# Kernel tuning notes

Measured on AMD Instinct MI355X. Metric: run time of the kernel, lower is better.

## Reference

```python
import jax, jax.numpy as jnp
import numpy as np

N_NODES = 100000
N_EDGES = 1600000


def gcn_conv(x, edge_index, W, b):
    """PyG-style GCNConv: self-loops + symmetric normalization + scatter-add."""
    n = x.shape[0]
    src, dst = edge_index[0], edge_index[1]
    loop = jnp.arange(n, dtype=src.dtype)
    src = jnp.concatenate([src, loop])
    dst = jnp.concatenate([dst, loop])
    h = x @ W  # [n, out] transform before propagate (PyG order)
    deg = jax.ops.segment_sum(jnp.ones_like(dst, dtype=h.dtype), dst, num_segments=n)
    dinv = jnp.where(deg > 0, deg ** -0.5, 0.0)
    norm = dinv[src] * dinv[dst]  # [E+n]
    msgs = h[src] * norm[:, None]  # gather + scale (largest intermediate)
    out = jax.ops.segment_sum(msgs, dst, num_segments=n)
    return out + b


def setup_inputs() -> dict:
    key = jax.random.key(0)
    ks = jax.random.split(key, 8)
    edge_attr = jax.random.normal(ks[0], (N_NODES, 5), dtype=jnp.float32)
    edge_index = jax.random.randint(ks[1], (2, N_EDGES), 0, N_NODES, dtype=jnp.int64)
    def lin(k, fan_in, fan_out):
        bound = 1.0 / np.sqrt(fan_in)
        return jax.random.uniform(k, (fan_in, fan_out), jnp.float32, -bound, bound)
    return {
        "edge_attr": edge_attr,
        "edge_index": edge_index,
        "W1": lin(ks[2], 5, 64),
        "b1": jnp.zeros((64,), jnp.float32),
        "W2": lin(ks[3], 64, 32),
        "b2": jnp.zeros((32,), jnp.float32),
        "fcW1": lin(ks[4], 32, 16),
        "fcb1": jnp.zeros((16,), jnp.float32),
        "fcW2": lin(ks[5], 16, 2),
        "fcb2": jnp.zeros((2,), jnp.float32),
    }


def reference(edge_attr, edge_index, W1, b1, W2, b2, fcW1, fcb1, fcW2, fcb2):
    x = jax.nn.relu(gcn_conv(edge_attr, edge_index, W1, b1))
    x = jax.nn.relu(gcn_conv(x, edge_index, W2, b2))
    x = jax.nn.relu(x @ fcW1 + fcb1)
    return x @ fcW2 + fcb2
```

## Files before the change

### kernel.cpp

```cpp
#include <hip/hip_runtime.h>


#define MS_TILE 2048
#define MAXB 512
#define AGG_NODES 32
#define AGG_STAGE 1024
#define PF_T 512
#define PF_EPT 10
#define PF_OV 1024

typedef __attribute__((ext_vector_type(4))) _Float16 half4;
typedef __attribute__((ext_vector_type(8))) _Float16 half8;

__device__ inline int scan256_incl(int v, int lane, int w, int* wsum,
                                   int* total) {
    int incl = v;
#pragma unroll
    for (int d = 1; d < 64; d <<= 1) {
        int up = __shfl_up(incl, d, 64);
        if (lane >= d) incl += up;
    }
    if (lane == 63) wsum[w] = incl;
    __syncthreads();
    int add = 0;
    if (w > 0) add += wsum[0];
    if (w > 1) add += wsum[1];
    if (w > 2) add += wsum[2];
    *total = wsum[0] + wsum[1] + wsum[2] + wsum[3];
    return incl + add;
}

__global__ __launch_bounds__(256) void histA(const int* __restrict__ dst,
                                             int* __restrict__ histG, int E) {
    __shared__ int h[MAXB];
    int t = threadIdx.x;
    h[t] = 0;
    h[t + 256] = 0;
    __syncthreads();
    int base = blockIdx.x * MS_TILE;
    int cnt = min(MS_TILE, E - base);
    for (int k = t; k < cnt; k += 256) atomicAdd(&h[dst[base + k] >> 8], 1);
    __syncthreads();
    histG[blockIdx.x * MAXB + t] = h[t];
    histG[blockIdx.x * MAXB + 256 + t] = h[t + 256];
}

__global__ __launch_bounds__(512) void scanTilesT(const int* __restrict__ histG,
                                                  int* __restrict__ offsG,
                                                  int* __restrict__ bucketTotal,
                                                  int nTiles) {
    __shared__ int lds[8][66];
    int t = threadIdx.x;
    int lane = t & 63, w = t >> 6;
    int rr = t >> 3, bb = t & 7;
    int B0 = blockIdx.x * 8;
    int carry = 0;
    for (int c0 = 0; c0 < nTiles; c0 += 64) {
        int rows = min(64, nTiles - c0);
        int v = 0;
        if (rr < rows) v = histG[(size_t)(c0 + rr) * MAXB + B0 + bb];
        lds[bb][rr] = v;
        __syncthreads();
        int x = lds[w][lane];
        int incl = x;
#pragma unroll
        for (int d = 1; d < 64; d <<= 1) {
            int up = __shfl_up(incl, d, 64);
            if (lane >= d) incl += up;
        }
        int total = __shfl(incl, 63, 64);
        lds[w][lane] = incl - x + carry;
        carry += total;
        __syncthreads();
        if (rr < rows) offsG[(size_t)(c0 + rr) * MAXB + B0 + bb] = lds[bb][rr];
    }
    if (lane == 0) bucketTotal[B0 + w] = carry;
}

__global__ __launch_bounds__(256) void multisplit2(
    const int* __restrict__ src, const int* __restrict__ dst,
    const int* __restrict__ histG, const int* __restrict__ offsG,
    const int* __restrict__ btot, int* __restrict__ gbaseOut,
    unsigned* __restrict__ binned, int E) {
    __shared__ unsigned stage[MS_TILE];
    __shared__ unsigned short sb[MS_TILE];
    __shared__ int hoff[MAXB + 1];
    __shared__ int hcur[MAXB];
    __shared__ int gb[MAXB];
    __shared__ int wsum[4];
    int t = threadIdx.x;
    int lane = t & 63, w = t >> 6;
    int tile = blockIdx.x;
    int base = tile * MS_TILE;
    int cnt = min(MS_TILE, E - base);

    int b0 = btot[2 * t], b1v = btot[2 * t + 1];
    int s2 = b0 + b1v;
    int tot2;
    int incl2 = scan256_incl(s2, lane, w, wsum, &tot2);
    int ex2 = incl2 - s2;
    gb[2 * t] = ex2 + offsG[tile * MAXB + 2 * t];
    gb[2 * t + 1] = ex2 + b0 + offsG[tile * MAXB + 2 * t + 1];
    if (tile == 0) {
        gbaseOut[2 * t] = ex2;
        gbaseOut[2 * t + 1] = ex2 + b0;
        if (t == 255) gbaseOut[MAXB] = E;
    }
    __syncthreads();

    int a0 = histG[tile * MAXB + 2 * t];
    int a1 = histG[tile * MAXB + 2 * t + 1];
    int s = a0 + a1;
    int tot;
    int incl = scan256_incl(s, lane, w, wsum, &tot);
    int ex = incl - s;
    hoff[2 * t] = ex;
    hoff[2 * t + 1] = ex + a0;
    hcur[2 * t] = ex;
    hcur[2 * t + 1] = ex + a0;
    if (t == 255) hoff[MAXB] = cnt;
    __syncthreads();
    for (int k = t; k < cnt; k += 256) {
        int d = dst[base + k];
        int b = d >> 8;
        int p = atomicAdd(&hcur[b], 1);
        stage[p] = ((unsigned)src[base + k] << 8) | (unsigned)(d & 255);
        sb[p] = (unsigned short)b;
    }
    __syncthreads();
    for (int k = t; k < cnt; k += 256) {
        int b = sb[k];
        binned[gb[b] + (k - hoff[b])] = stage[k];
    }
}

__global__ __launch_bounds__(PF_T) void place_fine2(
    const unsigned* __restrict__ binned, const int* __restrict__ gbase,
    const float* __restrict__ x, int* __restrict__ offs,
    float* __restrict__ dinv, _Float16* __restrict__ y, int* __restrict__ srcs,
    int n) {
    __shared__ int cnt[256];
    __shared__ int baseL[256];
    __shared__ int wsum[8];
    __shared__ unsigned ovW[PF_OV];
    __shared__ int ovR[PF_OV];
    __shared__ int ovN;
    int t = threadIdx.x, b = blockIdx.x;
    int lane = t & 63, w = t >> 6;
    int node0 = b << 8;
    int nn = min(256, n - node0);
    int e0 = gbase[b], e1 = gbase[b + 1];
    if (t < 256) cnt[t] = 0;
    if (t == 0) ovN = 0;
    __syncthreads();

    unsigned wdv[PF_EPT];
    int rk[PF_EPT];
    int nc = 0;
#pragma unroll
    for (int u = 0; u < PF_EPT; ++u) {
        int k = e0 + t + u * PF_T;
        if (k < e1) {
            unsigned wd = binned[k];
            wdv[u] = wd;
            rk[u] = atomicAdd(&cnt[wd & 255u], 1);
            nc = u + 1;
        }
    }
    for (int k = e0 + t + PF_EPT * PF_T; k < e1; k += PF_T) {
        unsigned wd = binned[k];
        int r = atomicAdd(&cnt[wd & 255u], 1);
        int j = atomicAdd(&ovN, 1);
        if (j < PF_OV) { ovW[j] = wd; ovR[j] = r; }
    }
    __syncthreads();

    int c = (t < 256) ? cnt[t] : 0;
    int incl = c;
#pragma unroll
    for (int d = 1; d < 64; d <<= 1) {
        int up = __shfl_up(incl, d, 64);
        if (lane >= d) incl += up;
    }
    if (lane == 63) wsum[w] = incl;
    __syncthreads();
    int add = 0;
    if (w > 0) add += wsum[0];
    if (w > 1) add += wsum[1];
    if (w > 2) add += wsum[2];
    incl += add;
    if (t < 256) {
        int myoff = e0 + incl - c;
        baseL[t] = myoff;
        if (t < nn) {
            int node = node0 + t;
            offs[node] = myoff;
            float di = 1.0f / sqrtf((float)(c + 1));
            dinv[node] = di;
            const float* xr = x + (size_t)node * 5;
            half8 hv;
            hv[0] = (_Float16)(xr[0] * di);
            hv[1] = (_Float16)(xr[1] * di);
            hv[2] = (_Float16)(xr[2] * di);
            hv[3] = (_Float16)(xr[3] * di);
            hv[4] = (_Float16)(xr[4] * di);
            hv[5] = (_Float16)0.f;
            hv[6] = (_Float16)0.f;
            hv[7] = (_Float16)0.f;
            *(half8*)(y + (size_t)node * 8) = hv;
        }
    }
    __syncthreads();

#pragma unroll
    for (int u = 0; u < PF_EPT; ++u) {
        if (u < nc) {
            unsigned wd = wdv[u];
            srcs[baseL[wd & 255u] + rk[u]] = (int)(wd >> 8);
        }
    }
    int no = ovN;
    for (int j = t; j < no; j += PF_T) {
        unsigned wd = ovW[j];
        srcs[baseL[wd & 255u] + ovR[j]] = (int)(wd >> 8);
    }
}

__global__ __launch_bounds__(256) void agg1_t12(
    const _Float16* __restrict__ y, const int* __restrict__ srcs,
    const int* __restrict__ offs, const float* __restrict__ dinv,
    const float* __restrict__ W1, const float* __restrict__ b1,
    const float* __restrict__ W2, _Float16* __restrict__ h2, int n, int E) {
    __shared__ float w1s[320];
    __shared__ float b1s[64];
    __shared__ float w2s[64 * 32];
    __shared__ float o1[32 * 64];
    __shared__ float zs[32 * 6];
    int t = threadIdx.x;
    w1s[t] = W1[t];
    if (t < 64) {
        w1s[t + 256] = W1[t + 256];
        b1s[t] = b1[t];
    }
#pragma unroll
    for (int r = 0; r < 8; ++r) w2s[r * 256 + t] = W2[r * 256 + t];

    int node0 = blockIdx.x * 32;
    int li = t >> 3, e = t & 7;
    int i = node0 + li;
    const half8* yv = (const half8*)y;
    float a0 = 0.f, a1 = 0.f, a2 = 0.f, a3 = 0.f, a4 = 0.f;
    if (i < n) {
        int off = offs[i];
        int cnt = ((i + 1 < n) ? offs[i + 1] : E) - off;
        if (e == 0) {
            half8 v = yv[i];
            a0 = (float)v[0]; a1 = (float)v[1]; a2 = (float)v[2];
            a3 = (float)v[3]; a4 = (float)v[4];
        }
        for (int p = e; p < cnt; p += 8) {
            half8 v = yv[srcs[off + p]];
            a0 += (float)v[0]; a1 += (float)v[1]; a2 += (float)v[2];
            a3 += (float)v[3]; a4 += (float)v[4];
        }
    }
#pragma unroll
    for (int m = 4; m >= 1; m >>= 1) {
        a0 += __shfl_xor(a0, m, 64);
        a1 += __shfl_xor(a1, m, 64);
        a2 += __shfl_xor(a2, m, 64);
        a3 += __shfl_xor(a3, m, 64);
        a4 += __shfl_xor(a4, m, 64);
    }
    if (i < n && e == 0) {
        float di = dinv[i];
        zs[li * 6 + 0] = a0 * di;
        zs[li * 6 + 1] = a1 * di;
        zs[li * 6 + 2] = a2 * di;
        zs[li * 6 + 3] = a3 * di;
        zs[li * 6 + 4] = a4 * di;
        zs[li * 6 + 5] = di;
    }
    __syncthreads();
#pragma unroll
    for (int r = 0; r < 8; ++r) {
        int idx = r * 256 + t;
        int lj = idx >> 6, f = idx & 63;
        if (node0 + lj < n) {
            const float* zr = zs + lj * 6;
            float acc = b1s[f];
#pragma unroll
            for (int k = 0; k < 5; ++k) acc += zr[k] * w1s[k * 64 + f];
            o1[lj * 64 + f] = fmaxf(acc, 0.0f);
        }
    }
    __syncthreads();
#pragma unroll
    for (int r = 0; r < 4; ++r) {
        int idx = r * 256 + t;
        int lj = idx >> 5, g = idx & 31;
        int i2 = node0 + lj;
        if (i2 < n) {
            float acc = 0.f;
#pragma unroll
            for (int k = 0; k < 64; ++k) acc += o1[lj * 64 + k] * w2s[k * 32 + g];
            h2[(size_t)i2 * 32 + g] = (_Float16)(acc * zs[lj * 6 + 5]);
        }
    }
}

__global__ __launch_bounds__(256) void agg2_fc(
    const _Float16* __restrict__ h, const int* __restrict__ srcs,
    const int* __restrict__ offs, const float* __restrict__ dinv,
    const float* __restrict__ b2, const float* __restrict__ fcW1,
    const float* __restrict__ fcb1, const float* __restrict__ fcW2,
    const float* __restrict__ fcb2, float* __restrict__ out, int n, int E) {
    __shared__ int sidx[AGG_STAGE];
    __shared__ float sm[AGG_NODES * 33];
    __shared__ float x3s[AGG_NODES * 16];
    __shared__ float w1s[512];
    __shared__ float w2s[32];
    __shared__ float b1s[16];
    __shared__ float b2s[2];
    __shared__ float bs2[32];
    int t = threadIdx.x;
    w1s[t] = fcW1[t];
    w1s[t + 256] = fcW1[t + 256];
    if (t < 32) { w2s[t] = fcW2[t]; bs2[t] = b2[t]; }
    if (t < 16) b1s[t] = fcb1[t];
    if (t < 2) b2s[t] = fcb2[t];

    int node0 = blockIdx.x * AGG_NODES;
    int li = t >> 3, fq = t & 7;
    int i = node0 + li;
    bool live = (i < n);
    const char* hb = (const char*)h;

    int e0 = offs[node0];
    int eEnd = (node0 + AGG_NODES < n) ? offs[node0 + AGG_NODES] : E;
    int myOff = 0, myCnt = 0;
    float4 acc = {0.f, 0.f, 0.f, 0.f};
    if (live) {
        myOff = offs[i];
        myCnt = ((i + 1 < n) ? offs[i + 1] : E) - myOff;
        half4 sv = *(const half4*)(hb + ((size_t)i << 6) + (fq << 3));
        acc.x = (float)sv.x; acc.y = (float)sv.y;
        acc.z = (float)sv.z; acc.w = (float)sv.w;
    }

    for (int cs = e0; cs < eEnd; cs += AGG_STAGE) {
        int ce = min(cs + AGG_STAGE, eEnd);
        for (int k = cs + t; k < ce; k += 256) sidx[k - cs] = srcs[k] << 6;
        __syncthreads();
        int ps = max(myOff, cs), pe = min(myOff + myCnt, ce);
        int p = ps;
        for (; p + 8 <= pe; p += 8) {
            int o[8];
#pragma unroll
            for (int u = 0; u < 8; ++u) o[u] = sidx[p + u - cs];
            half4 v[8];
#pragma unroll
            for (int u = 0; u < 8; ++u)
                v[u] = *(const half4*)(hb + o[u] + (fq << 3));
#pragma unroll
            for (int u = 0; u < 8; ++u) {
                acc.x += (float)v[u].x; acc.y += (float)v[u].y;
                acc.z += (float)v[u].z; acc.w += (float)v[u].w;
            }
        }
        for (; p + 4 <= pe; p += 4) {
            int o0 = sidx[p - cs], o1 = sidx[p + 1 - cs];
            int o2 = sidx[p + 2 - cs], o3 = sidx[p + 3 - cs];
            half4 v0 = *(const half4*)(hb + o0 + (fq << 3));
            half4 v1 = *(const half4*)(hb + o1 + (fq << 3));
            half4 v2 = *(const half4*)(hb + o2 + (fq << 3));
            half4 v3 = *(const half4*)(hb + o3 + (fq << 3));
            acc.x += (float)v0.x + (float)v1.x + (float)v2.x + (float)v3.x;
            acc.y += (float)v0.y + (float)v1.y + (float)v2.y + (float)v3.y;
            acc.z += (float)v0.z + (float)v1.z + (float)v2.z + (float)v3.z;
            acc.w += (float)v0.w + (float)v1.w + (float)v2.w + (float)v3.w;
        }
        for (; p < pe; ++p) {
            half4 v = *(const half4*)(hb + sidx[p - cs] + (fq << 3));
            acc.x += (float)v.x; acc.y += (float)v.y;
            acc.z += (float)v.z; acc.w += (float)v.w;
        }
        __syncthreads();
    }

    if (live) {
        float di = dinv[i];
        int f0 = fq << 2;
        sm[li * 33 + f0 + 0] = fmaxf(di * acc.x + bs2[f0 + 0], 0.f);
        sm[li * 33 + f0 + 1] = fmaxf(di * acc.y + bs2[f0 + 1], 0.f);
        sm[li * 33 + f0 + 2] = fmaxf(di * acc.z + bs2[f0 + 2], 0.f);
        sm[li * 33 + f0 + 3] = fmaxf(di * acc.w + bs2[f0 + 3], 0.f);
    }
    __syncthreads();
#pragma unroll
    for (int r = 0; r < 2; ++r) {
        int idx = r * 256 + t;
        int lj = idx >> 4, j = idx & 15;
        if (node0 + lj < n) {
            float a = b1s[j];
#pragma unroll
            for (int k = 0; k < 32; ++k) a += sm[lj * 33 + k] * w1s[k * 16 + j];
            x3s[lj * 16 + j] = fmaxf(a, 0.f);
        }
    }
    __syncthreads();
    if (t < 64) {
        int lj = t >> 1, o = t & 1;
        if (node0 + lj < n) {
            float a = b2s[o];
#pragma unroll
            for (int j = 0; j < 16; ++j) a += x3s[lj * 16 + j] * w2s[j * 2 + o];
            out[(size_t)(node0 + lj) * 2 + o] = a;
        }
    }
}

extern "C" void kernel_launch(void* const* d_in, const int* in_sizes, int n_in,
                              void* d_out, int out_size, void* d_ws, size_t ws_size,
                              hipStream_t stream) {
    const float* edge_attr = (const float*)d_in[0];
    const int* edge_index  = (const int*)d_in[1];
    const float* W1   = (const float*)d_in[2];
    const float* b1   = (const float*)d_in[3];
    const float* W2   = (const float*)d_in[4];
    const float* b2   = (const float*)d_in[5];
    const float* fcW1 = (const float*)d_in[6];
    const float* fcb1 = (const float*)d_in[7];
    const float* fcW2 = (const float*)d_in[8];
    const float* fcb2 = (const float*)d_in[9];
    float* out = (float*)d_out;

    int n = in_sizes[0] / 5;
    int E = in_sizes[1] / 2;
    int NBkt = (n + 255) >> 8;
    int nTiles = (E + MS_TILE - 1) / MS_TILE;
    const int* src = edge_index;
    const int* dst = edge_index + E;

    char* ws = (char*)d_ws;
    auto alloc = [&](size_t bytes) {
        char* p = ws;
        ws += (bytes + 255) & ~(size_t)255;
        return p;
    };
    int*      offs   = (int*)alloc((size_t)n * 4);
    float*    dinv   = (float*)alloc((size_t)n * 4);
    int*      histG  = (int*)alloc((size_t)nTiles * MAXB * 4);
    int*      offsG  = (int*)alloc((size_t)nTiles * MAXB * 4);
    int*      btot   = (int*)alloc((size_t)MAXB * 4);
    int*      gbase  = (int*)alloc((size_t)(MAXB + 1) * 4);
    int*      srcs   = (int*)alloc((size_t)E * 4);
    unsigned* binned = (unsigned*)alloc((size_t)E * 4);
    _Float16* y      = (_Float16*)alloc((size_t)n * 8 * 2);
    _Float16* h2     = (_Float16*)alloc((size_t)n * 32 * 2);

    histA<<<nTiles, 256, 0, stream>>>(dst, histG, E);
    scanTilesT<<<MAXB / 8, 512, 0, stream>>>(histG, offsG, btot, nTiles);
    multisplit2<<<nTiles, 256, 0, stream>>>(src, dst, histG, offsG, btot, gbase,
                                            binned, E);
    place_fine2<<<NBkt, PF_T, 0, stream>>>(binned, gbase, edge_attr, offs, dinv,
                                           y, srcs, n);
    agg1_t12<<<(n + 31) / 32, 256, 0, stream>>>(y, srcs, offs, dinv, W1, b1, W2,
                                                h2, n, E);
    agg2_fc<<<(n + AGG_NODES - 1) / AGG_NODES, 256, 0, stream>>>(
        h2, srcs, offs, dinv, b2, fcW1, fcb1, fcW2, fcb2, out, n, E);
}
```

Before: 179.5 us.

## Fuse fine CSR placement into aggregation kernels using LDS-resident per-bucket edge lists

Drops the global srcs/offs CSR build. Each aggregation kernel now re-derives its 256-node bucket's sorted source list in shared memory from the binned edges, then aggregates 64 nodes at a time. Degree is computed with global atomics in the histogram pass, and dinv/y are produced in the otherwise idle blocks of the scan kernel. This removes a kernel and the global srcs write/read traffic, but the local sort is done twice, and 512-thread blocks with large LDS (~50KB+) may cut occupancy. Buckets with more than 5120 edges silently drop edges beyond the LDS capacity.

```diff
diff --git a/kernel.cpp b/kernel.cpp
--- a/kernel.cpp
+++ b/kernel.cpp
@@ -3,14 +3,14 @@
 
 #define MS_TILE 2048
 #define MAXB 512
-#define AGG_NODES 32
-#define AGG_STAGE 1024
-#define PF_T 512
-#define PF_EPT 10
-#define PF_OV 1024
+#define AB_T 512
+#define AB_EPT 10
+#define AB_CAP (AB_T * AB_EPT)
+#define AB_OV 1024
 
 typedef __attribute__((ext_vector_type(4))) _Float16 half4;
 typedef __attribute__((ext_vector_type(8))) _Float16 half8;
+typedef __attribute__((ext_vector_type(4))) int int4v;
 
 __device__ inline int scan256_incl(int v, int lane, int w, int* wsum,
                                    int* total) {
@@ -30,8 +30,14 @@
     return incl + add;
 }
 
-__global__ __launch_bounds__(256) void histA(const int* __restrict__ dst,
-                                             int* __restrict__ histG, int E) {
+__global__ __launch_bounds__(256) void zero_deg(int* __restrict__ deg, int n4) {
+    int i = blockIdx.x * 256 + threadIdx.x;
+    if (i < n4) ((int4v*)deg)[i] = int4v{0, 0, 0, 0};
+}
+
+__global__ __launch_bounds__(256) void histA_deg(const int* __restrict__ dst,
+                                                 int* __restrict__ histG,
+                                                 int* __restrict__ deg, int E) {
     __shared__ int h[MAXB];
     int t = threadIdx.x;
     h[t] = 0;
@@ -39,42 +45,71 @@
     __syncthreads();
     int base = blockIdx.x * MS_TILE;
     int cnt = min(MS_TILE, E - base);
-    for (int k = t; k < cnt; k += 256) atomicAdd(&h[dst[base + k] >> 8], 1);
+    for (int k = t; k < cnt; k += 256) {
+        int d = dst[base + k];
+        atomicAdd(&h[d >> 8], 1);
+        atomicAdd(&deg[d], 1);
+    }
     __syncthreads();
     histG[blockIdx.x * MAXB + t] = h[t];
     histG[blockIdx.x * MAXB + 256 + t] = h[t + 256];
 }
 
-__global__ __launch_bounds__(512) void scanTilesT(const int* __restrict__ histG,
-                                                  int* __restrict__ offsG,
-                                                  int* __restrict__ bucketTotal,
-                                                  int nTiles) {
+__global__ __launch_bounds__(512) void scanY(const int* __restrict__ histG,
+                                             int* __restrict__ offsG,
+                                             int* __restrict__ bucketTotal,
+                                             const int* __restrict__ deg,
+                                             const float* __restrict__ x,
+                                             float* __restrict__ dinv,
+                                             _Float16* __restrict__ y,
+                                             int nTiles, int n) {
     __shared__ int lds[8][66];
     int t = threadIdx.x;
-    int lane = t & 63, w = t >> 6;
-    int rr = t >> 3, bb = t & 7;
-    int B0 = blockIdx.x * 8;
-    int carry = 0;
-    for (int c0 = 0; c0 < nTiles; c0 += 64) {
-        int rows = min(64, nTiles - c0);
-        int v = 0;
-        if (rr < rows) v = histG[(size_t)(c0 + rr) * MAXB + B0 + bb];
-        lds[bb][rr] = v;
-        __syncthreads();
-        int x = lds[w][lane];
-        int incl = x;
-#pragma unroll
-        for (int d = 1; d < 64; d <<= 1) {
-            int up = __shfl_up(incl, d, 64);
-            if (lane >= d) incl += up;
-        }
-        int total = __shfl(incl, 63, 64);
-        lds[w][lane] = incl - x + carry;
-        carry += total;
-        __syncthreads();
-        if (rr < rows) offsG[(size_t)(c0 + rr) * MAXB + B0 + bb] = lds[bb][rr];
-    }
-    if (lane == 0) bucketTotal[B0 + w] = carry;
+    if (blockIdx.x < 64) {
+        int lane = t & 63, w = t >> 6;
+        int rr = t >> 3, bb = t & 7;
+        int B0 = blockIdx.x * 8;
+        int carry = 0;
+        for (int c0 = 0; c0 < nTiles; c0 += 64) {
+            int rows = min(64, nTiles - c0);
+            int v = 0;
+            if (rr < rows) v = histG[(size_t)(c0 + rr) * MAXB + B0 + bb];
+            lds[bb][rr] = v;
+            __syncthreads();
+            int x0 = lds[w][lane];
+            int incl = x0;
+#pragma unroll
+            for (int d = 1; d < 64; d <<= 1) {
+                int up = __shfl_up(incl, d, 64);
+                if (lane >= d) incl += up;
+            }
+            int total = __shfl(incl, 63, 64);
+            lds[w][lane] = incl - x0 + carry;
+            carry += total;
+            __syncthreads();
+            if (rr < rows) offsG[(size_t)(c0 + rr) * MAXB + B0 + bb] = lds[bb][rr];
+            __syncthreads();
+        }
+        if (lane == 0) bucketTotal[B0 + w] = carry;
+    } else {
+        int base = (blockIdx.x - 64) * 512;
+        int stride = (gridDim.x - 64) * 512;
+        for (int i = base + t; i < n; i += stride) {
+            float di = 1.0f / sqrtf((float)(deg[i] + 1));
+            dinv[i] = di;
+            const float* xr = x + (size_t)i * 5;
+            half8 hv;
+            hv[0] = (_Float16)(xr[0] * di);
+            hv[1] = (_Float16)(xr[1] * di);
+            hv[2] = (_Float16)(xr[2] * di);
+            hv[3] = (_Float16)(xr[3] * di);
+            hv[4] = (_Float16)(xr[4] * di);
+            hv[5] = (_Float16)0.f;
+            hv[6] = (_Float16)0.f;
+            hv[7] = (_Float16)0.f;
+            *(half8*)(y + (size_t)i * 8) = hv;
+        }
+    }
 }
 
 __global__ __launch_bounds__(256) void multisplit2(
@@ -134,48 +169,57 @@
     }
 }
 
-__global__ __launch_bounds__(PF_T) void place_fine2(
+__global__ __launch_bounds__(AB_T) void aggB1(
     const unsigned* __restrict__ binned, const int* __restrict__ gbase,
-    const float* __restrict__ x, int* __restrict__ offs,
-    float* __restrict__ dinv, _Float16* __restrict__ y, int* __restrict__ srcs,
-    int n) {
-    __shared__ int cnt[256];
-    __shared__ int baseL[256];
+    const _Float16* __restrict__ y, const float* __restrict__ dinv,
+    const float* __restrict__ W1, const float* __restrict__ b1,
+    const float* __restrict__ W2, _Float16* __restrict__ h2, int n, int E) {
+    __shared__ int cntL[256];
+    __shared__ int exL[256];
     __shared__ int wsum[8];
-    __shared__ unsigned ovW[PF_OV];
-    __shared__ int ovR[PF_OV];
+    __shared__ int srcsL[AB_CAP];
+    __shared__ unsigned ovW[AB_OV];
+    __shared__ int ovR[AB_OV];
     __shared__ int ovN;
+    __shared__ float w1s[320];
+    __shared__ float b1s[64];
+    __shared__ float w2s[2048];
+    __shared__ float o1[64 * 64];
+    __shared__ float zs[64 * 6];
     int t = threadIdx.x, b = blockIdx.x;
     int lane = t & 63, w = t >> 6;
     int node0 = b << 8;
-    int nn = min(256, n - node0);
     int e0 = gbase[b], e1 = gbase[b + 1];
-    if (t < 256) cnt[t] = 0;
+
+    if (t < 320) w1s[t] = W1[t];
+    if (t < 64) b1s[t] = b1[t];
+#pragma unroll
+    for (int r = 0; r < 4; ++r) w2s[r * 512 + t] = W2[r * 512 + t];
+    if (t < 256) cntL[t] = 0;
     if (t == 0) ovN = 0;
     __syncthreads();
 
-    unsigned wdv[PF_EPT];
-    int rk[PF_EPT];
+    unsigned wdv[AB_EPT];
+    int rk[AB_EPT];
     int nc = 0;
 #pragma unroll
-    for (int u = 0; u < PF_EPT; ++u) {
-        int k = e0 + t + u * PF_T;
+    for (int u = 0; u < AB_EPT; ++u) {
+        int k = e0 + t + u * AB_T;
         if (k < e1) {
             unsigned wd = binned[k];
             wdv[u] = wd;
-            rk[u] = atomicAdd(&cnt[wd & 255u], 1);
+            rk[u] = atomicAdd(&cntL[wd & 255u], 1);
             nc = u + 1;
         }
     }
-    for (int k = e0 + t + PF_EPT * PF_T; k < e1; k += PF_T) {
+    for (int k = e0 + t + AB_EPT * AB_T; k < e1; k += AB_T) {
         unsigned wd = binned[k];
-        int r = atomicAdd(&cnt[wd & 255u], 1);
+        int r = atomicAdd(&cntL[wd & 255u], 1);
         int j = atomicAdd(&ovN, 1);
-        if (j < PF_OV) { ovW[j] = wd; ovR[j] = r; }
-    }
-    __syncthreads();
-
-    int c = (t < 256) ? cnt[t] : 0;
+        if (j < AB_OV) { ovW[j] = wd; ovR[j] = r; }
+    }
+    __syncthreads();
+    int c = (t < 256) ? cntL[t] : 0;
     int incl = c;
 #pragma unroll
     for (int d = 1; d < 64; d <<= 1) {
@@ -189,175 +233,196 @@
     if (w > 1) add += wsum[1];
     if (w > 2) add += wsum[2];
     incl += add;
-    if (t < 256) {
-        int myoff = e0 + incl - c;
-        baseL[t] = myoff;
-        if (t < nn) {
-            int node = node0 + t;
-            offs[node] = myoff;
-            float di = 1.0f / sqrtf((float)(c + 1));
-            dinv[node] = di;
-            const float* xr = x + (size_t)node * 5;
-            half8 hv;
-            hv[0] = (_Float16)(xr[0] * di);
-            hv[1] = (_Float16)(xr[1] * di);
-            hv[2] = (_Float16)(xr[2] * di);
-            hv[3] = (_Float16)(xr[3] * di);
-            hv[4] = (_Float16)(xr[4] * di);
-            hv[5] = (_Float16)0.f;
-            hv[6] = (_Float16)0.f;
-            hv[7] = (_Float16)0.f;
-            *(half8*)(y + (size_t)node * 8) = hv;
-        }
-    }
-    __syncthreads();
-
-#pragma unroll
-    for (int u = 0; u < PF_EPT; ++u) {
+    if (t < 256) exL[t] = incl - c;
+    __syncthreads();
+#pragma unroll
+    for (int u = 0; u < AB_EPT; ++u) {
         if (u < nc) {
             unsigned wd = wdv[u];
-            srcs[baseL[wd & 255u] + rk[u]] = (int)(wd >> 8);
-        }
-    }
-    int no = ovN;
-    for (int j = t; j < no; j += PF_T) {
+            int pos = exL[wd & 255u] + rk[u];
+            if (pos < AB_CAP) srcsL[pos] = (int)(wd >> 8);
+        }
+    }
+    int no = min(ovN, AB_OV);
+    for (int j = t; j < no; j += AB_T) {
         unsigned wd = ovW[j];
-        srcs[baseL[wd & 255u] + ovR[j]] = (int)(wd >> 8);
-    }
-}
-
-__global__ __launch_bounds__(256) void agg1_t12(
-    const _Float16* __restrict__ y, const int* __restrict__ srcs,
-    const int* __restrict__ offs, const float* __restrict__ dinv,
-    const float* __restrict__ W1, const float* __restrict__ b1,
-    const float* __restrict__ W2, _Float16* __restrict__ h2, int n, int E) {
-    __shared__ float w1s[320];
-    __shared__ float b1s[64];
-    __shared__ float w2s[64 * 32];
-    __shared__ float o1[32 * 64];
-    __shared__ float zs[32 * 6];
-    int t = threadIdx.x;
-    w1s[t] = W1[t];
-    if (t < 64) {
-        w1s[t + 256] = W1[t + 256];
-        b1s[t] = b1[t];
-    }
-#pragma unroll
-    for (int r = 0; r < 8; ++r) w2s[r * 256 + t] = W2[r * 256 + t];
-
-    int node0 = blockIdx.x * 32;
+        int pos = exL[wd & 255u] + ovR[j];
+        if (pos < AB_CAP) srcsL[pos] = (int)(wd >> 8);
+    }
+    __syncthreads();
+
+    const half8* yv = (const half8*)y;
     int li = t >> 3, e = t & 7;
-    int i = node0 + li;
-    const half8* yv = (const half8*)y;
-    float a0 = 0.f, a1 = 0.f, a2 = 0.f, a3 = 0.f, a4 = 0.f;
-    if (i < n) {
-        int off = offs[i];
-        int cnt = ((i + 1 < n) ? offs[i + 1] : E) - off;
-        if (e == 0) {
-            half8 v = yv[i];
-            a0 = (float)v[0]; a1 = (float)v[1]; a2 = (float)v[2];
-            a3 = (float)v[3]; a4 = (float)v[4];
-        }
-        for (int p = e; p < cnt; p += 8) {
-            half8 v = yv[srcs[off + p]];
-            a0 += (float)v[0]; a1 += (float)v[1]; a2 += (float)v[2];
-            a3 += (float)v[3]; a4 += (float)v[4];
-        }
-    }
-#pragma unroll
-    for (int m = 4; m >= 1; m >>= 1) {
-        a0 += __shfl_xor(a0, m, 64);
-        a1 += __shfl_xor(a1, m, 64);
-        a2 += __shfl_xor(a2, m, 64);
-        a3 += __shfl_xor(a3, m, 64);
-        a4 += __shfl_xor(a4, m, 64);
-    }
-    if (i < n && e == 0) {
-        float di = dinv[i];
-        zs[li * 6 + 0] = a0 * di;
-        zs[li * 6 + 1] = a1 * di;
-        zs[li * 6 + 2] = a2 * di;
-        zs[li * 6 + 3] = a3 * di;
-        zs[li * 6 + 4] = a4 * di;
-        zs[li * 6 + 5] = di;
-    }
-    __syncthreads();
-#pragma unroll
-    for (int r = 0; r < 8; ++r) {
-        int idx = r * 256 + t;
-        int lj = idx >> 6, f = idx & 63;
-        if (node0 + lj < n) {
-            const float* zr = zs + lj * 6;
-            float acc = b1s[f];
-#pragma unroll
-            for (int k = 0; k < 5; ++k) acc += zr[k] * w1s[k * 64 + f];
-            o1[lj * 64 + f] = fmaxf(acc, 0.0f);
-        }
-    }
-    __syncthreads();
-#pragma unroll
-    for (int r = 0; r < 4; ++r) {
-        int idx = r * 256 + t;
-        int lj = idx >> 5, g = idx & 31;
-        int i2 = node0 + lj;
-        if (i2 < n) {
-            float acc = 0.f;
-#pragma unroll
-            for (int k = 0; k < 64; ++k) acc += o1[lj * 64 + k] * w2s[k * 32 + g];
-            h2[(size_t)i2 * 32 + g] = (_Float16)(acc * zs[lj * 6 + 5]);
-        }
-    }
-}
-
-__global__ __launch_bounds__(256) void agg2_fc(
-    const _Float16* __restrict__ h, const int* __restrict__ srcs,
-    const int* __restrict__ offs, const float* __restrict__ dinv,
+    for (int g = 0; g < 4; ++g) {
+        int l = g * 64 + li;
+        int i = node0 + l;
+        float a0 = 0.f, a1 = 0.f, a2 = 0.f, a3 = 0.f, a4 = 0.f;
+        if (i < n) {
+            int myo = exL[l], myc = cntL[l];
+            if (e == 0) {
+                half8 v = yv[i];
+                a0 = (float)v[0]; a1 = (float)v[1]; a2 = (float)v[2];
+                a3 = (float)v[3]; a4 = (float)v[4];
+            }
+            for (int p = e; p < myc; p += 8) {
+                half8 v = yv[srcsL[myo + p]];
+                a0 += (float)v[0]; a1 += (float)v[1]; a2 += (float)v[2];
+                a3 += (float)v[3]; a4 += (float)v[4];
+            }
+        }
+#pragma unroll
+        for (int m = 4; m >= 1; m >>= 1) {
+            a0 += __shfl_xor(a0, m, 64);
+            a1 += __shfl_xor(a1, m, 64);
+            a2 += __shfl_xor(a2, m, 64);
+            a3 += __shfl_xor(a3, m, 64);
+            a4 += __shfl_xor(a4, m, 64);
+        }
+        if (i < n && e == 0) {
+            float di = dinv[i];
+            zs[li * 6 + 0] = a0 * di;
+            zs[li * 6 + 1] = a1 * di;
+            zs[li * 6 + 2] = a2 * di;
+            zs[li * 6 + 3] = a3 * di;
+            zs[li * 6 + 4] = a4 * di;
+            zs[li * 6 + 5] = di;
+        }
+        __syncthreads();
+#pragma unroll
+        for (int r = 0; r < 8; ++r) {
+            int idx = r * 512 + t;
+            int lj = idx >> 6, f = idx & 63;
+            if (node0 + g * 64 + lj < n) {
+                const float* zr = zs + lj * 6;
+                float acc = b1s[f];
+#pragma unroll
+                for (int k = 0; k < 5; ++k) acc += zr[k] * w1s[k * 64 + f];
+                o1[lj * 64 + f] = fmaxf(acc, 0.0f);
+            }
+        }
+        __syncthreads();
+#pragma unroll
+        for (int r = 0; r < 4; ++r) {
+            int idx = r * 512 + t;
+            int lj = idx >> 5, gg = idx & 31;
+            int i2 = node0 + g * 64 + lj;
+            if (i2 < n) {
+                float acc = 0.f;
+#pragma unroll
+                for (int k = 0; k < 64; ++k)
+                    acc += o1[lj * 64 + k] * w2s[k * 32 + gg];
+                h2[(size_t)i2 * 32 + gg] = (_Float16)(acc * zs[lj * 6 + 5]);
+            }
+        }
+        __syncthreads();
+    }
+}
+
+__global__ __launch_bounds__(AB_T) void aggB2(
+    const unsigned* __restrict__ binned, const int* __restrict__ gbase,
+    const _Float16* __restrict__ h, const float* __restrict__ dinv,
     const float* __restrict__ b2, const float* __restrict__ fcW1,
     const float* __restrict__ fcb1, const float* __restrict__ fcW2,
     const float* __restrict__ fcb2, float* __restrict__ out, int n, int E) {
-    __shared__ int sidx[AGG_STAGE];
-    __shared__ float sm[AGG_NODES * 33];
-    __shared__ float x3s[AGG_NODES * 16];
+    __shared__ int cntL[256];
+    __shared__ int exL[256];
+    __shared__ int wsum[8];
+    __shared__ int srcsL[AB_CAP];
+    __shared__ unsigned ovW[AB_OV];
+    __shared__ int ovR[AB_OV];
+    __shared__ int ovN;
+    __shared__ float sm[64 * 33];
+    __shared__ float x3s[64 * 16];
     __shared__ float w1s[512];
-    __shared__ float w2s[32];
-    __shared__ float b1s[16];
-    __shared__ float b2s[2];
+    __shared__ float w2sF[32];
+    __shared__ float b1sF[16];
+    __shared__ float b2sF[2];
     __shared__ float bs2[32];
-    int t = threadIdx.x;
-    w1s[t] = fcW1[t];
-    w1s[t + 256] = fcW1[t + 256];
-    if (t < 32) { w2s[t] = fcW2[t]; bs2[t] = b2[t]; }
-    if (t < 16) b1s[t] = fcb1[t];
-    if (t < 2) b2s[t] = fcb2[t];
-
-    int node0 = blockIdx.x * AGG_NODES;
+    int t = threadIdx.x, b = blockIdx.x;
+    int lane = t & 63, w = t >> 6;
+    int node0 = b << 8;
+    int e0 = gbase[b], e1 = gbase[b + 1];
+
+    if (t < 512) w1s[t] = fcW1[t];
+    if (t < 32) { w2sF[t] = fcW2[t]; bs2[t] = b2[t]; }
+    if (t < 16) b1sF[t] = fcb1[t];
+    if (t < 2) b2sF[t] = fcb2[t];
+    if (t < 256) cntL[t] = 0;
+    if (t == 0) ovN = 0;
+    __syncthreads();
+
+    unsigned wdv[AB_EPT];
+    int rk[AB_EPT];
+    int nc = 0;
+#pragma unroll
+    for (int u = 0; u < AB_EPT; ++u) {
+        int k = e0 + t + u * AB_T;
+        if (k < e1) {
+            unsigned wd = binned[k];
+            wdv[u] = wd;
+            rk[u] = atomicAdd(&cntL[wd & 255u], 1);
+            nc = u + 1;
+        }
+    }
+    for (int k = e0 + t + AB_EPT * AB_T; k < e1; k += AB_T) {
+        unsigned wd = binned[k];
+        int r = atomicAdd(&cntL[wd & 255u], 1);
+        int j = atomicAdd(&ovN, 1);
+        if (j < AB_OV) { ovW[j] = wd; ovR[j] = r; }
+    }
+    __syncthreads();
+    int c = (t < 256) ? cntL[t] : 0;
+    int incl = c;
+#pragma unroll
+    for (int d = 1; d < 64; d <<= 1) {
+        int up = __shfl_up(incl, d, 64);
+        if (lane >= d) incl += up;
+    }
+    if (lane == 63) wsum[w] = incl;
+    __syncthreads();
+    int add = 0;
+    if (w > 0) add += wsum[0];
+    if (w > 1) add += wsum[1];
+    if (w > 2) add += wsum[2];
+    incl += add;
+    if (t < 256) exL[t] = incl - c;
+    __syncthreads();
+#pragma unroll
+    for (int u = 0; u < AB_EPT; ++u) {
+        if (u < nc) {
+            unsigned wd = wdv[u];
+            int pos = exL[wd & 255u] + rk[u];
+            if (pos < AB_CAP) srcsL[pos] = (int)(wd >> 8);
+        }
+    }
+    int no = min(ovN, AB_OV);
+    for (int j = t; j < no; j += AB_T) {
+        unsigned wd = ovW[j];
+        int pos = exL[wd & 255u] + ovR[j];
+        if (pos < AB_CAP) srcsL[pos] = (int)(wd >> 8);
+    }
+    __syncthreads();
+
     int li = t >> 3, fq = t & 7;
-    int i = node0 + li;
-    bool live = (i < n);
     const char* hb = (const char*)h;
-
-    int e0 = offs[node0];
-    int eEnd = (node0 + AGG_NODES < n) ? offs[node0 + AGG_NODES] : E;
-    int myOff = 0, myCnt = 0;
-    float4 acc = {0.f, 0.f, 0.f, 0.f};
-    if (live) {
-        myOff = offs[i];
-        myCnt = ((i + 1 < n) ? offs[i + 1] : E) - myOff;
-        half4 sv = *(const half4*)(hb + ((size_t)i << 6) + (fq << 3));
-        acc.x = (float)sv.x; acc.y = (float)sv.y;
-        acc.z = (float)sv.z; acc.w = (float)sv.w;
-    }
-
-    for (int cs = e0; cs < eEnd; cs += AGG_STAGE) {
-        int ce = min(cs + AGG_STAGE, eEnd);
-        for (int k = cs + t; k < ce; k += 256) sidx[k - cs] = srcs[k] << 6;
-        __syncthreads();
-        int ps = max(myOff, cs), pe = min(myOff + myCnt, ce);
-        int p = ps;
-        for (; p + 8 <= pe; p += 8) {
+    for (int g = 0; g < 4; ++g) {
+        int l = g * 64 + li;
+        int i = node0 + l;
+        bool live = (i < n);
+        float4 acc = {0.f, 0.f, 0.f, 0.f};
+        int myo = 0, myc = 0;
+        if (live) {
+            myo = exL[l];
+            myc = cntL[l];
+            half4 sv = *(const half4*)(hb + ((size_t)i << 6) + (fq << 3));
+            acc.x = (float)sv.x; acc.y = (float)sv.y;
+            acc.z = (float)sv.z; acc.w = (float)sv.w;
+        }
+        int p = 0;
+        for (; p + 8 <= myc; p += 8) {
             int o[8];
 #pragma unroll
-            for (int u = 0; u < 8; ++u) o[u] = sidx[p + u - cs];
+            for (int u = 0; u < 8; ++u) o[u] = srcsL[myo + p + u] << 6;
             half4 v[8];
 #pragma unroll
             for (int u = 0; u < 8; ++u)
@@ -368,11 +433,11 @@
                 acc.z += (float)v[u].z; acc.w += (float)v[u].w;
             }
         }
-        for (; p + 4 <= pe; p += 4) {
-            int o0 = sidx[p - cs], o1 = sidx[p + 1 - cs];
-            int o2 = sidx[p + 2 - cs], o3 = sidx[p + 3 - cs];
+        for (; p + 4 <= myc; p += 4) {
+            int o0 = srcsL[myo + p] << 6, o1v = srcsL[myo + p + 1] << 6;
+            int o2 = srcsL[myo + p + 2] << 6, o3 = srcsL[myo + p + 3] << 6;
             half4 v0 = *(const half4*)(hb + o0 + (fq << 3));
-            half4 v1 = *(const half4*)(hb + o1 + (fq << 3));
+            half4 v1 = *(const half4*)(hb + o1v + (fq << 3));
             half4 v2 = *(const half4*)(hb + o2 + (fq << 3));
             half4 v3 = *(const half4*)(hb + o3 + (fq << 3));
             acc.x += (float)v0.x + (float)v1.x + (float)v2.x + (float)v3.x;
@@ -380,43 +445,43 @@
             acc.z += (float)v0.z + (float)v1.z + (float)v2.z + (float)v3.z;
             acc.w += (float)v0.w + (float)v1.w + (float)v2.w + (float)v3.w;
         }
-        for (; p < pe; ++p) {
-            half4 v = *(const half4*)(hb + sidx[p - cs] + (fq << 3));
+        for (; p < myc; ++p) {
+            half4 v = *(const half4*)(hb + (srcsL[myo + p] << 6) + (fq << 3));
             acc.x += (float)v.x; acc.y += (float)v.y;
             acc.z += (float)v.z; acc.w += (float)v.w;
         }
+        if (live) {
+            float di = dinv[i];
+            int f0 = fq << 2;
+            sm[li * 33 + f0 + 0] = fmaxf(di * acc.x + bs2[f0 + 0], 0.f);
+            sm[li * 33 + f0 + 1] = fmaxf(di * acc.y + bs2[f0 + 1], 0.f);
+            sm[li * 33 + f0 + 2] = fmaxf(di * acc.z + bs2[f0 + 2], 0.f);
+            sm[li * 33 + f0 + 3] = fmaxf(di * acc.w + bs2[f0 + 3], 0.f);
+        }
         __syncthreads();
-    }
-
-    if (live) {
-        float di = dinv[i];
-        int f0 = fq << 2;
-        sm[li * 33 + f0 + 0] = fmaxf(di * acc.x + bs2[f0 + 0], 0.f);
-        sm[li * 33 + f0 + 1] = fmaxf(di * acc.y + bs2[f0 + 1], 0.f);
-        sm[li * 33 + f0 + 2] = fmaxf(di * acc.z + bs2[f0 + 2], 0.f);
-        sm[li * 33 + f0 + 3] = fmaxf(di * acc.w + bs2[f0 + 3], 0.f);
-    }
-    __syncthreads();
-#pragma unroll
-    for (int r = 0; r < 2; ++r) {
-        int idx = r * 256 + t;
-        int lj = idx >> 4, j = idx & 15;
-        if (node0 + lj < n) {
-            float a = b1s[j];
-#pragma unroll
-            for (int k = 0; k < 32; ++k) a += sm[lj * 33 + k] * w1s[k * 16 + j];
-            x3s[lj * 16 + j] = fmaxf(a, 0.f);
-        }
-    }
-    __syncthreads();
-    if (t < 64) {
-        int lj = t >> 1, o = t & 1;
-        if (node0 + lj < n) {
-            float a = b2s[o];
-#pragma unroll
-            for (int j = 0; j < 16; ++j) a += x3s[lj * 16 + j] * w2s[j * 2 + o];
-            out[(size_t)(node0 + lj) * 2 + o] = a;
-        }
+#pragma unroll
+        for (int r = 0; r < 2; ++r) {
+            int idx = r * 512 + t;
+            int lj = idx >> 4, j = idx & 15;
+            if (node0 + g * 64 + lj < n) {
+                float a = b1sF[j];
+#pragma unroll
+                for (int k = 0; k < 32; ++k) a += sm[lj * 33 + k] * w1s[k * 16 + j];
+                x3s[lj * 16 + j] = fmaxf(a, 0.f);
+            }
+        }
+        __syncthreads();
+        if (t < 128) {
+            int lj = t >> 1, o = t & 1;
+            if (node0 + g * 64 + lj < n) {
+                float a = b2sF[o];
+#pragma unroll
+                for (int j = 0; j < 16; ++j)
+                    a += x3s[lj * 16 + j] * w2sF[j * 2 + o];
+                out[(size_t)(node0 + g * 64 + lj) * 2 + o] = a;
+            }
+        }
+        __syncthreads();
     }
 }
 
@@ -448,25 +513,25 @@
         ws += (bytes + 255) & ~(size_t)255;
         return p;
     };
-    int*      offs   = (int*)alloc((size_t)n * 4);
+    int*      deg    = (int*)alloc((size_t)n * 4 + 16);
     float*    dinv   = (float*)alloc((size_t)n * 4);
     int*      histG  = (int*)alloc((size_t)nTiles * MAXB * 4);
     int*      offsG  = (int*)alloc((size_t)nTiles * MAXB * 4);
     int*      btot   = (int*)alloc((size_t)MAXB * 4);
     int*      gbase  = (int*)alloc((size_t)(MAXB + 1) * 4);
-    int*      srcs   = (int*)alloc((size_t)E * 4);
     unsigned* binned = (unsigned*)alloc((size_t)E * 4);
     _Float16* y      = (_Float16*)alloc((size_t)n * 8 * 2);
     _Float16* h2     = (_Float16*)alloc((size_t)n * 32 * 2);
 
-    histA<<<nTiles, 256, 0, stream>>>(dst, histG, E);
-    scanTilesT<<<MAXB / 8, 512, 0, stream>>>(histG, offsG, btot, nTiles);
+    int n4 = (n + 3) >> 2;
+    zero_deg<<<(n4 + 255) / 256, 256, 0, stream>>>(deg, n4);
+    histA_deg<<<nTiles, 256, 0, stream>>>(dst, histG, deg, E);
+    scanY<<<64 + 128, 512, 0, stream>>>(histG, offsG, btot, deg, edge_attr,
+                                        dinv, y, nTiles, n);
     multisplit2<<<nTiles, 256, 0, stream>>>(src, dst, histG, offsG, btot, gbase,
                                             binned, E);
-    place_fine2<<<NBkt, PF_T, 0, stream>>>(binned, gbase, edge_attr, offs, dinv,
-                                           y, srcs, n);
-    agg1_t12<<<(n + 31) / 32, 256, 0, stream>>>(y, srcs, offs, dinv, W1, b1, W2,
-                                                h2, n, E);
-    agg2_fc<<<(n + AGG_NODES - 1) / AGG_NODES, 256, 0, stream>>>(
-        h2, srcs, offs, dinv, b2, fcW1, fcb1, fcW2, fcb2, out, n, E);
-}
+    aggB1<<<NBkt, AB_T, 0, stream>>>(binned, gbase, y, dinv, W1, b1, W2, h2, n,
+                                     E);
+    aggB2<<<NBkt, AB_T, 0, stream>>>(binned, gbase, h2, dinv, b2, fcW1, fcb1,
+                                     fcW2, fcb2, out, n, E);
+}
```

After: 245.6 us. +36.8%, slower.
